# Performance work log

Hardware: AMD Instinct MI355X
Metric: run time of the kernel (lower is better)

## Reference

```python
import jax, jax.numpy as jnp
import numpy as np

EPS = 1e-8
TAU = 10.0
SCALE = 1.0
PH, PW = 5, 5  # patch_size; stride == patch_size (module default)
CX, CY = PH // 2, PW // 2


def _split_into_patches(x):
    """[B, C, H, W] -> [B, C, L, ph, pw] with non-overlapping ph x pw patches
    (stride == patch size, matching the module's default patch_stride)."""
    B, C, H, W = x.shape
    Hp, Wp = H // PH, W // PW
    x = x[:, :, : Hp * PH, : Wp * PW].reshape(B, C, Hp, PH, Wp, PW)
    x = x.transpose(0, 1, 2, 4, 3, 5)  # [B, C, Hp, Wp, ph, pw]
    return x.reshape(B, C, Hp * Wp, PH, PW)


def setup_inputs() -> dict:
    key = jax.random.key(0)
    k1, k2 = jax.random.split(key)
    seg_feat = jax.random.normal(k1, (4, 64, 512, 512), dtype=jnp.float32)
    dep_true = jax.random.uniform(k2, (4, 1, 512, 512), dtype=jnp.float32) * 80.0
    return {"seg_feat": seg_feat, "dep_true": dep_true}


def reference(seg_feat, dep_true):
    seg_feat = seg_feat.astype(jnp.float32)
    dep_true = dep_true.astype(jnp.float32)

    # --- depth branch (no_grad in the original) ---
    dep_patch = _split_into_patches(dep_true)[:, 0]          # [B, L, ph, pw]
    dep_valid = dep_patch > EPS
    dep_center = dep_patch[:, :, CX, CY][:, :, None, None]   # [B, L, 1, 1]
    dep_diff = jnp.abs(dep_center - dep_patch)               # [B, L, ph, pw]

    # --- segmentation branch ---
    seg_patch = _split_into_patches(seg_feat)                # [B, C, L, ph, pw]
    seg_center = seg_patch[:, :, :, CX, CY][:, :, :, None, None]
    seg_sq = jnp.sum((seg_center - seg_patch) ** 2, axis=1)  # [B, L, ph, pw] = seg_diff**2

    # exp(-seg_diff**2) == exp(-seg_sq); avoids sqrt in the differentiable path
    loss = jnp.exp(-dep_diff / TAU) * jnp.exp(-seg_sq)

    # --- mask (no_grad in the original) ---
    seg_diff = jnp.sqrt(seg_sq)
    mask = (dep_diff > EPS) & (seg_diff > EPS) & dep_valid
    mask = mask.at[:, :, CX, CY].set(False)

    # masked_select(...).mean()
    n = jnp.maximum(jnp.sum(mask), 1)
    mean = jnp.sum(jnp.where(mask, loss, 0.0)) / n.astype(loss.dtype)
    return mean * SCALE
```

## Files before the change

kernel.cpp:

```cpp
#include <hip/hip_runtime.h>
#include <math.h>


#define EPSF 1e-8f
#define PH 5
#define HPATCH 102
#define HH 512
#define WW 512
#define CC 64


__global__ __launch_bounds__(320) void dgp_main(const float* __restrict__ seg,
                                                const float* __restrict__ dep,
                                                float* __restrict__ ws) {
  const int bid   = blockIdx.x;
  const int chunk = bid & 1;
  const int hp    = (bid >> 1) % HPATCH;
  const int b     = (bid >> 1) / HPATCH;
  const int h0    = hp * PH;
  const int hc    = h0 + 2;

  const int wp0 = chunk ? 51 : 0;
  const int nwp = chunk ? 51 : 52;

  __shared__ float s_cent[52 * 65];
  __shared__ float s_depc[52];
  __shared__ float s_red[10];

  const int tid = threadIdx.x;
  const long seg_b = (long)b * CC * HH * WW;

  const int ntot = nwp * CC + nwp;
  for (int i = tid; i < ntot; i += 320) {
    if (i < nwp * CC) {
      int wpl = i % nwp;
      int c   = i / nwp;
      int wcol = (wp0 + wpl) * PH + 2;
      s_cent[wpl * 65 + c] = seg[seg_b + ((long)c * HH + hc) * WW + wcol];
    } else {
      int wpl  = i - nwp * CC;
      int wcol = (wp0 + wpl) * PH + 2;
      s_depc[wpl] = dep[((long)b * HH + hc) * WW + wcol];
    }
  }
  __syncthreads();

  const int row  = tid >> 6;
  const int lane = tid & 63;
  const int col0 = chunk * 256 + lane * 4;

  int w0 = min((col0 + 0) / PH - wp0, nwp - 1);
  int w1 = min((col0 + 1) / PH - wp0, nwp - 1);
  int w2 = min((col0 + 2) / PH - wp0, nwp - 1);
  int w3 = min((col0 + 3) / PH - wp0, nwp - 1);

  const float* cb0 = s_cent + w0 * 65;
  const float* cb1 = s_cent + w1 * 65;
  const float* cb2 = s_cent + w2 * 65;
  const float* cb3 = s_cent + w3 * 65;

  float acc0 = 0.f, acc1 = 0.f, acc2 = 0.f, acc3 = 0.f;
  const float* p = seg + seg_b + (long)(h0 + row) * WW + col0;

#pragma unroll 4
  for (int c = 0; c < CC; ++c) {
    float4 v = *(const float4*)(p + (long)c * (HH * WW));
    float c0 = cb0[c], c1 = cb1[c], c2 = cb2[c], c3 = cb3[c];
    float d0 = c0 - v.x;
    float d1 = c1 - v.y;
    float d2 = c2 - v.z;
    float d3 = c3 - v.w;
    acc0 = fmaf(d0, d0, acc0);
    acc1 = fmaf(d1, d1, acc1);
    acc2 = fmaf(d2, d2, acc2);
    acc3 = fmaf(d3, d3, acc3);
  }

  float4 dv = *(const float4*)(dep + ((long)b * HH + h0 + row) * WW + col0);
  float dvals[4] = {dv.x, dv.y, dv.z, dv.w};
  float accs[4]  = {acc0, acc1, acc2, acc3};
  int wls[4]     = {w0, w1, w2, w3};

  float lsum = 0.f, lcnt = 0.f;
#pragma unroll
  for (int j = 0; j < 4; ++j) {
    int col = col0 + j;
    if (col < 510) {
      float dval = dvals[j];
      float dd   = fabsf(s_depc[wls[j]] - dval);
      float ssq  = accs[j];
      bool is_center = (row == 2) && (col % 5 == 2);
      bool m = (dd > EPSF) && (ssq > EPSF * EPSF) && (dval > EPSF) && !is_center;
      if (m) {
        lsum += expf(-(dd * 0.1f + ssq));
        lcnt += 1.f;
      }
    }
  }

#pragma unroll
  for (int off = 32; off > 0; off >>= 1) {
    lsum += __shfl_down(lsum, off, 64);
    lcnt += __shfl_down(lcnt, off, 64);
  }
  if (lane == 0) {
    s_red[row]     = lsum;
    s_red[5 + row] = lcnt;
  }
  __syncthreads();
  if (tid == 0) {
    float a = 0.f, n = 0.f;
#pragma unroll
    for (int w = 0; w < 5; ++w) {
      a += s_red[w];
      n += s_red[5 + w];
    }
    atomicAdd(&ws[0], a);
    atomicAdd(&ws[1], n);
  }
}

__global__ void dgp_final(const float* __restrict__ ws, float* __restrict__ out) {
  out[0] = ws[0] / fmaxf(ws[1], 1.0f);
}

extern "C" void kernel_launch(void* const* d_in, const int* in_sizes, int n_in,
                              void* d_out, int out_size, void* d_ws, size_t ws_size,
                              hipStream_t stream) {
  const float* seg = (const float*)d_in[0];
  const float* dep = (const float*)d_in[1];
  float* out = (float*)d_out;
  float* ws  = (float*)d_ws;

  hipMemsetAsync(d_ws, 0, 2 * sizeof(float), stream);

  const int nblocks = 4 * HPATCH * 2;
  dgp_main<<<dim3(nblocks), dim3(320), 0, stream>>>(seg, dep, ws);
  dgp_final<<<1, 1, 0, stream>>>(ws, out);
}
```

Baseline: 373.4 us.

## Split each patch row into four column quarters with float2 loads per thread

Each block now covers a 128-column quarter of a patch row instead of half, doubling the block count and halving per-thread work from four columns (float4) to two (float2). The centre-pixel gather is rewritten so 32-lane groups stride over channels, and the exp uses the fast __expf intrinsic. The aim is more blocks and more waves in flight to hide memory latency on a bandwidth-bound reduction. The costs are narrower loads, more repeated centre gathers per row, and twice as many atomics.

Result: faster. 365.5 us (-2.1%).

```diff
diff --git a/kernel.cpp b/kernel.cpp
--- a/kernel.cpp
+++ b/kernel.cpp
@@ -8,91 +8,84 @@
 #define HH 512
 #define WW 512
 #define CC 64
-
+#define HW (HH * WW)
 
 __global__ __launch_bounds__(320) void dgp_main(const float* __restrict__ seg,
                                                 const float* __restrict__ dep,
                                                 float* __restrict__ ws) {
-  const int bid   = blockIdx.x;
-  const int chunk = bid & 1;
-  const int hp    = (bid >> 1) % HPATCH;
-  const int b     = (bid >> 1) / HPATCH;
-  const int h0    = hp * PH;
-  const int hc    = h0 + 2;
+  const int bid = blockIdx.x;
+  const int q   = bid & 3;
+  const int hp  = (bid >> 2) % HPATCH;
+  const int b   = (bid >> 2) / HPATCH;
+  const int h0  = hp * PH;
+  const int hc  = h0 + 2;
+  const int qbase = q * 128;
 
-  const int wp0 = chunk ? 51 : 0;
-  const int nwp = chunk ? 51 : 52;
+  const int wp0   = qbase / PH;
+  const int wpend = min((qbase + 127) / PH, HPATCH - 1);
+  const int nwp   = wpend - wp0 + 1;
 
-  __shared__ float s_cent[52 * 65];
-  __shared__ float s_depc[52];
+  __shared__ float s_cent[27 * 65];
+  __shared__ float s_depc[27];
   __shared__ float s_red[10];
 
   const int tid = threadIdx.x;
-  const long seg_b = (long)b * CC * HH * WW;
+  const long seg_b = (long)b * CC * HW;
 
-  const int ntot = nwp * CC + nwp;
-  for (int i = tid; i < ntot; i += 320) {
-    if (i < nwp * CC) {
-      int wpl = i % nwp;
-      int c   = i / nwp;
-      int wcol = (wp0 + wpl) * PH + 2;
-      s_cent[wpl * 65 + c] = seg[seg_b + ((long)c * HH + hc) * WW + wcol];
-    } else {
-      int wpl  = i - nwp * CC;
-      int wcol = (wp0 + wpl) * PH + 2;
-      s_depc[wpl] = dep[((long)b * HH + hc) * WW + wcol];
+  {
+    const int grp = tid >> 5;
+    const int wpl = tid & 31;
+    if (wpl < nwp) {
+      const long base = seg_b + (long)hc * WW + (wp0 + wpl) * PH + 2;
+      for (int c = grp; c < CC; c += 10) {
+        s_cent[wpl * 65 + c] = seg[base + (long)c * HW];
+      }
+    }
+    if (tid < nwp) {
+      s_depc[tid] = dep[((long)b * HH + hc) * WW + (wp0 + tid) * PH + 2];
     }
   }
   __syncthreads();
 
   const int row  = tid >> 6;
   const int lane = tid & 63;
-  const int col0 = chunk * 256 + lane * 4;
+  const int col0 = qbase + lane * 2;
 
-  int w0 = min((col0 + 0) / PH - wp0, nwp - 1);
+  int w0 = min(col0 / PH - wp0, nwp - 1);
   int w1 = min((col0 + 1) / PH - wp0, nwp - 1);
-  int w2 = min((col0 + 2) / PH - wp0, nwp - 1);
-  int w3 = min((col0 + 3) / PH - wp0, nwp - 1);
 
   const float* cb0 = s_cent + w0 * 65;
   const float* cb1 = s_cent + w1 * 65;
-  const float* cb2 = s_cent + w2 * 65;
-  const float* cb3 = s_cent + w3 * 65;
 
-  float acc0 = 0.f, acc1 = 0.f, acc2 = 0.f, acc3 = 0.f;
+  float acc0 = 0.f, acc1 = 0.f;
   const float* p = seg + seg_b + (long)(h0 + row) * WW + col0;
 
-#pragma unroll 4
+#pragma unroll 8
   for (int c = 0; c < CC; ++c) {
-    float4 v = *(const float4*)(p + (long)c * (HH * WW));
-    float c0 = cb0[c], c1 = cb1[c], c2 = cb2[c], c3 = cb3[c];
-    float d0 = c0 - v.x;
-    float d1 = c1 - v.y;
-    float d2 = c2 - v.z;
-    float d3 = c3 - v.w;
+    float2 v = *(const float2*)(p + (long)c * HW);
+    float d0 = cb0[c] - v.x;
+    float d1 = cb1[c] - v.y;
     acc0 = fmaf(d0, d0, acc0);
     acc1 = fmaf(d1, d1, acc1);
-    acc2 = fmaf(d2, d2, acc2);
-    acc3 = fmaf(d3, d3, acc3);
   }
 
-  float4 dv = *(const float4*)(dep + ((long)b * HH + h0 + row) * WW + col0);
-  float dvals[4] = {dv.x, dv.y, dv.z, dv.w};
-  float accs[4]  = {acc0, acc1, acc2, acc3};
-  int wls[4]     = {w0, w1, w2, w3};
+  float2 dv = *(const float2*)(dep + ((long)b * HH + h0 + row) * WW + col0);
+  float dvals[2] = {dv.x, dv.y};
+  float accs[2]  = {acc0, acc1};
+  int wls[2]     = {w0, w1};
 
   float lsum = 0.f, lcnt = 0.f;
 #pragma unroll
-  for (int j = 0; j < 4; ++j) {
+  for (int j = 0; j < 2; ++j) {
     int col = col0 + j;
     if (col < 510) {
       float dval = dvals[j];
       float dd   = fabsf(s_depc[wls[j]] - dval);
       float ssq  = accs[j];
-      bool is_center = (row == 2) && (col % 5 == 2);
+      bool is_center = (row == 2) && (col % PH == 2);
       bool m = (dd > EPSF) && (ssq > EPSF * EPSF) && (dval > EPSF) && !is_center;
       if (m) {
-        lsum += expf(-(dd * 0.1f + ssq));
+        lsum += __expf(-(dd * 0.1f + ssq));
         lcnt += 1.f;
       }
     }
@@ -134,7 +127,7 @@
 
   hipMemsetAsync(d_ws, 0, 2 * sizeof(float), stream);
 
-  const int nblocks = 4 * HPATCH * 2;
+  const int nblocks = 4 * HPATCH * 4;
   dgp_main<<<dim3(nblocks), dim3(320), 0, stream>>>(seg, dep, ws);
   dgp_final<<<1, 1, 0, stream>>>(ws, out);
 }
```
